# Performance work log

Hardware: AMD Instinct MI355X
Metric: run time of the kernel (lower is better)

Reference implementation:

```python
import jax, jax.numpy as jnp
import numpy as np

CLASSES = 256
SUPERCLASSES = 16
CLASS_FACTOR = CLASSES // SUPERCLASSES
HEIGHT = 448
WIDTH = 160
BATCH = 1
CH_IN = 128
CH_R0 = 256
CH_R1 = 8


def _leaky(v):
    return jnp.where(v >= 0, v, 0.01 * v)


def _grouped1x1(x, W, b):
    # x: (B, H, Cin, W_sp); W: (H, Cout, Cin); b: (H, Cout)
    return jnp.einsum('bhcw,hoc->bhow', x, W) + b[None, :, :, None]


def setup_inputs() -> dict:
    key = jax.random.key(0)
    ks = jax.random.split(key, 16)
    s = 0.05
    return {
        'x_in': jax.random.normal(ks[0], (BATCH, CH_IN, HEIGHT, WIDTH), jnp.float32),
        'W_cl1': jax.random.normal(ks[1], (HEIGHT, 128, CH_IN), jnp.float32) * s,
        'b_cl1': jax.random.normal(ks[2], (HEIGHT, 128), jnp.float32) * s,
        'W_cl2': jax.random.normal(ks[3], (HEIGHT, 128, 128), jnp.float32) * s,
        'b_cl2': jax.random.normal(ks[4], (HEIGHT, 128), jnp.float32) * s,
        'W_cl3': jax.random.normal(ks[5], (HEIGHT, 128, 128), jnp.float32) * s,
        'b_cl3': jax.random.normal(ks[6], (HEIGHT, 128), jnp.float32) * s,
        'W_cl4': jax.random.normal(ks[7], (HEIGHT, CLASSES + 1, 128), jnp.float32) * s,
        'b_cl4': jax.random.normal(ks[8], (HEIGHT, CLASSES + 1), jnp.float32) * s,
        'W_reg1': jax.random.normal(ks[9], (HEIGHT, CH_R0, CH_IN), jnp.float32) * s,
        'b_reg1': jax.random.normal(ks[10], (HEIGHT, CH_R0), jnp.float32) * s,
        'W_cm2': jax.random.normal(ks[11], (SUPERCLASSES * HEIGHT, CH_R0, CH_R1), jnp.float32) * s,
        'b_cm2': jax.random.normal(ks[12], (SUPERCLASSES * HEIGHT, CH_R1), jnp.float32) * s,
        'W_cm3': jax.random.normal(ks[13], (CLASSES * HEIGHT, CH_R1, 1), jnp.float32) * s,
        'b_cm3': jax.random.normal(ks[14], (CLASSES * HEIGHT, 1), jnp.float32) * s,
    }


def reference(x_in, W_cl1, b_cl1, W_cl2, b_cl2, W_cl3, b_cl3, W_cl4, b_cl4,
              W_reg1, b_reg1, W_cm2, b_cm2, W_cm3, b_cm3):
    B, C, H, Wd = x_in.shape
    x = x_in.transpose(0, 2, 1, 3)  # (B, H, C, W) == grouped-conv layout
    x_r = _leaky(_grouped1x1(x, W_reg1, b_reg1))  # (B, H, CH_R0, W)
    # classification branch
    h = _leaky(_grouped1x1(x, W_cl1, b_cl1))
    h = _leaky(_grouped1x1(h, W_cl2, b_cl2))
    h = _leaky(_grouped1x1(h, W_cl3, b_cl3))
    h = _grouped1x1(h, W_cl4, b_cl4)  # (B, H, CLASSES+1, W)
    logits = h.transpose(0, 2, 1, 3)  # (B, CLASSES+1, H, W)
    cls = logits[:, :CLASSES]
    mask = _leaky(logits[:, -1:])  # (B, 1, H, W)
    inds = jnp.argmax(cls, axis=1)[:, None]  # (B, 1, H, W)
    offs = jnp.arange(H)[None, None, :, None]
    # NOTE: original flattens indices in (b, h, w) order...
    inds_r = (inds + offs * CLASSES).reshape(-1).astype(jnp.int32)
    inds_sc = (inds // CLASS_FACTOR + offs * SUPERCLASSES).reshape(-1).astype(jnp.int32)
    # ...while CondMul input rows come in (b, w, h) order (faithful to torch code).
    xr_rows = x_r.transpose(0, 3, 1, 2).reshape(-1, CH_R0)  # (B*W*H, CH_R0)
    y = _leaky(jnp.einsum('nc,nco->no', xr_rows, W_cm2[inds_sc]) + b_cm2[inds_sc])
    r = jnp.einsum('nc,nco->no', y, W_cm3[inds_r]) + b_cm3[inds_r]  # (N, 1)
    r = r.reshape(B, Wd, H, 1).transpose(0, 3, 2, 1)  # (B, 1, H, W)
    x_real = (inds.astype(jnp.float32) + r) * (1.0 / CLASSES)
    return x_real, mask
```

## Files before the change

### kernel.cpp

```cpp
#include <hip/hip_runtime.h>
#include <hip/hip_bf16.h>

#define HH 448
#define WW 160
#define NPIX (HH*WW)

typedef unsigned long long u64;
typedef _Float16 h8 __attribute__((ext_vector_type(8)));
typedef _Float16 h4 __attribute__((ext_vector_type(4)));
typedef float f32x4 __attribute__((ext_vector_type(4)));

#define MFMA16(A,B,C) __builtin_amdgcn_mfma_f32_16x16x32_f16(A,B,C,0,0,0)
#define LO_SCALE 4096.0f
#define LO_INV   (1.0f/4096.0f)

__device__ __forceinline__ float leaky(float v) { return v >= 0.f ? v : 0.01f * v; }

__device__ __forceinline__ u64 packKey(float m, int r) {
    unsigned u = __float_as_uint(m);
    u = (u & 0x80000000u) ? ~u : (u | 0x80000000u);
    return ((u64)u << 32) | (unsigned)(255 - r);
}

__device__ __forceinline__ _Float16 splitHi(float v) { return (_Float16)v; }
__device__ __forceinline__ _Float16 splitLo(float v, _Float16 hi) {
    return (_Float16)((v - (float)hi) * LO_SCALE);
}

__device__ __forceinline__ void cvtA(const float4& v0, const float4& v1, h8& ah, h8& al) {
    const float v[8] = {v0.x,v0.y,v0.z,v0.w,v1.x,v1.y,v1.z,v1.w};
#pragma unroll
    for (int j = 0; j < 8; ++j) {
        const _Float16 hi = splitHi(v[j]);
        ah[j] = hi;
        al[j] = splitLo(v[j], hi);
    }
}

__device__ __forceinline__ void gemmPass(const _Float16* lah, const _Float16* lal,
                                         const float* __restrict__ Wp,
                                         int lrow, int lg, int col0,
                                         f32x4 aH[5], f32x4 aL[5])
{
    const f32x4 zero = {0.f, 0.f, 0.f, 0.f};
#pragma unroll
    for (int c = 0; c < 5; ++c) { aH[c] = zero; aL[c] = zero; }

    const float* wb = Wp + lrow * 128 + lg * 8;
    float4 ca0 = *(const float4*)(wb);
    float4 ca1 = *(const float4*)(wb + 4);
    float4 cb0 = *(const float4*)(wb + 32);
    float4 cb1 = *(const float4*)(wb + 36);

    const int ub = col0 + lrow;

#pragma unroll 1
    for (int s = 0; s < 4; s += 2) {
        const int sa = (s + 2) & 3, sb = (s + 3) & 3;
        float4 na0 = *(const float4*)(wb + sa * 32);
        float4 na1 = *(const float4*)(wb + sa * 32 + 4);
        float4 nb0 = *(const float4*)(wb + sb * 32);
        float4 nb1 = *(const float4*)(wb + sb * 32 + 4);

        h8 Ah, Al;
        cvtA(ca0, ca1, Ah, Al);
        {
            const int gg = (s << 2) + lg;
#pragma unroll
            for (int c = 0; c < 5; ++c) {
                const int u = gg * 160 + ub + (c << 4);
                const h8 Bh = *(const h8*)(lah + (u << 3));
                const h8 Bl = *(const h8*)(lal + (u << 3));
                aH[c] = MFMA16(Ah, Bh, aH[c]);
                aL[c] = MFMA16(Ah, Bl, aL[c]);
                aL[c] = MFMA16(Al, Bh, aL[c]);
            }
        }
        cvtA(cb0, cb1, Ah, Al);
        {
            const int gg = ((s + 1) << 2) + lg;
#pragma unroll
            for (int c = 0; c < 5; ++c) {
                const int u = gg * 160 + ub + (c << 4);
                const h8 Bh = *(const h8*)(lah + (u << 3));
                const h8 Bl = *(const h8*)(lal + (u << 3));
                aH[c] = MFMA16(Ah, Bh, aH[c]);
                aL[c] = MFMA16(Ah, Bl, aL[c]);
                aL[c] = MFMA16(Al, Bh, aL[c]);
            }
        }
        ca0 = na0; ca1 = na1; cb0 = nb0; cb1 = nb1;
    }
}

__global__ __launch_bounds__(1024, 4) void kA(
    const float* __restrict__ x_in,
    const float* __restrict__ Wcl1, const float* __restrict__ bcl1,
    const float* __restrict__ Wcl2, const float* __restrict__ bcl2,
    const float* __restrict__ Wcl3, const float* __restrict__ bcl3,
    const float* __restrict__ Wcl4, const float* __restrict__ bcl4,
    const float* __restrict__ Wreg1, const float* __restrict__ breg1,
    __hip_bfloat16* __restrict__ xr, int* __restrict__ ind, float* __restrict__ out)
{
    __shared__ alignas(16) _Float16 lah[16 * 160 * 8];
    __shared__ alignas(16) _Float16 lal[16 * 160 * 8];
    u64* argb = reinterpret_cast<u64*>(lah);

    const int h = blockIdx.x;
    const int t = threadIdx.x;
    const int wvid = t >> 6;
    const int l = t & 63;
    const int lrow = l & 15, lg = l >> 4;
    const int rt = wvid >> 1;
    const int ch = wvid & 1;
    const int col0 = ch * 80;
    const int trb = rt * 16;

#pragma unroll 1
    for (int k = 0; k < 3; ++k) {
        const int id = t + (k << 10);
        if (id < 2560) {
            const int g = id / 160, col = id - g * 160;
            float v[8];
#pragma unroll
            for (int j = 0; j < 8; ++j)
                v[j] = x_in[(size_t)(g * 8 + j) * 71680 + h * 160 + col];
            h8 hh, ll;
#pragma unroll
            for (int j = 0; j < 8; ++j) {
                const _Float16 hi = splitHi(v[j]);
                hh[j] = hi;
                ll[j] = splitLo(v[j], hi);
            }
            const int u = g * 160 + col;
            *(h8*)(lah + (u << 3)) = hh;
            *(h8*)(lal + (u << 3)) = ll;
        }
    }
    __syncthreads();

    {
        const float* W1 = Wreg1 + (size_t)h * 32768;
        const float* b1 = breg1 + h * 256;
#pragma unroll 1
        for (int p = 0; p < 2; ++p) {
            const int rowOff = (p << 7) + trb;
            f32x4 aH[5], aL[5];
            gemmPass(lah, lal, W1 + rowOff * 128, lrow, lg, col0, aH, aL);
            const int r0 = rowOff + (lg << 2);
            const float4 bb = *(const float4*)&b1[r0];
#pragma unroll
            for (int c = 0; c < 5; ++c) {
                const int col = col0 + (c << 4) + lrow;
                alignas(8) unsigned short us[4];
#pragma unroll
                for (int r = 0; r < 4; ++r) {
                    const float a = aH[c][r] + aL[c][r] * LO_INV + ((const float*)&bb)[r];
                    __hip_bfloat16 bv = __float2bfloat16(leaky(a));
                    us[r] = *(const unsigned short*)&bv;
                }
                *(uint2*)(xr + (((size_t)(h * 160 + col)) << 8) + r0) = *(const uint2*)us;
            }
        }
    }

#pragma unroll 1
    for (int L = 0; L < 3; ++L) {
        const float* W = (L == 0) ? Wcl1 + (size_t)h * 16384
                       : (L == 1) ? Wcl2 + (size_t)h * 16384
                                  : Wcl3 + (size_t)h * 16384;
        const float* b = (L == 0) ? bcl1 + (h << 7)
                       : (L == 1) ? bcl2 + (h << 7)
                                  : bcl3 + (h << 7);
        f32x4 aH[5], aL[5];
        gemmPass(lah, lal, W + trb * 128, lrow, lg, col0, aH, aL);
        const int r0 = trb + (lg << 2);
        const float4 bb = *(const float4*)&b[r0];
        float nv[5][4];
#pragma unroll
        for (int c = 0; c < 5; ++c)
#pragma unroll
            for (int r = 0; r < 4; ++r)
                nv[c][r] = leaky(aH[c][r] + aL[c][r] * LO_INV + ((const float*)&bb)[r]);
        __syncthreads();
        {
            const int g = r0 >> 3, off = r0 & 7;
#pragma unroll
            for (int c = 0; c < 5; ++c) {
                const int col = col0 + (c << 4) + lrow;
                h4 wh, wl;
#pragma unroll
                for (int r = 0; r < 4; ++r) {
                    const _Float16 hi = splitHi(nv[c][r]);
                    wh[r] = hi;
                    wl[r] = splitLo(nv[c][r], hi);
                }
                *(h4*)(lah + ((g * 160 + col) << 3) + off) = wh;
                *(h4*)(lal + ((g * 160 + col) << 3) + off) = wl;
            }
        }
        __syncthreads();
    }

    if (t < 160) {
        const float* Wm = Wcl4 + (size_t)h * 32896 + 32768;
        float accm = 0.f;
#pragma unroll 2
        for (int g = 0; g < 16; ++g) {
            const h8 hv = *(const h8*)(lah + ((g * 160 + t) << 3));
            const h8 lv = *(const h8*)(lal + ((g * 160 + t) << 3));
            const float4 w0 = *(const float4*)&Wm[g * 8];
            const float4 w1 = *(const float4*)&Wm[g * 8 + 4];
            const float wv[8] = {w0.x,w0.y,w0.z,w0.w,w1.x,w1.y,w1.z,w1.w};
#pragma unroll
            for (int j = 0; j < 8; ++j)
                accm = fmaf(wv[j], (float)hv[j] + (float)lv[j] * LO_INV, accm);
        }
        out[NPIX + h * 160 + t] = leaky(accm + bcl4[h * 257 + 256]);
    }

    float mv[5]; int mr[5];
    {
        const float* W4 = Wcl4 + (size_t)h * 32896;
        const float* b4 = bcl4 + h * 257;
#pragma unroll
        for (int c = 0; c < 5; ++c) { mv[c] = -3.4e38f; mr[c] = 0; }
#pragma unroll 1
        for (int p = 0; p < 2; ++p) {
            const int rowOff = (p << 7) + trb;
            f32x4 aH[5], aL[5];
            gemmPass(lah, lal, W4 + rowOff * 128, lrow, lg, col0, aH, aL);
            const int r0 = rowOff + (lg << 2);
            const float4 bb = *(const float4*)&b4[r0];
#pragma unroll
            for (int c = 0; c < 5; ++c)
#pragma unroll
                for (int r = 0; r < 4; ++r) {
                    const float a = aH[c][r] + aL[c][r] * LO_INV + ((const float*)&bb)[r];
                    if (a > mv[c]) { mv[c] = a; mr[c] = r0 + r; }
                }
        }
    }
    __syncthreads();
    if (t < 160) argb[t] = 0ull;
    __syncthreads();
#pragma unroll
    for (int c = 0; c < 5; ++c)
        atomicMax(&argb[col0 + (c << 4) + lrow], packKey(mv[c], mr[c]));
    __syncthreads();

    if (t < 160) {
        const u64 kk = argb[t];
        ind[h * 160 + t] = 255 - (int)(kk & 0xFFu);
    }
}

__global__ __launch_bounds__(256) void kB(
    const __hip_bfloat16* __restrict__ xr, const int* __restrict__ ind,
    const float* __restrict__ Wcm2, const float* __restrict__ bcm2,
    const float* __restrict__ Wcm3, const float* __restrict__ bcm3,
    float* __restrict__ out)
{
    const int wid = (int)((blockIdx.x * blockDim.x + threadIdx.x) >> 6);
    const int lane = threadIdx.x & 63;

#pragma unroll 1
    for (int k = 0; k < 10; ++k) {
        const int n = wid * 10 + k;
        const int h_o = n % HH, w_o = n / HH;
        const int h_i = n / WW, w_i = n % WW;
        const int ig = ind[h_i * WW + w_i];
        const int sc = (ig >> 4) + (h_i << 4);
        const int rr = ig + (h_i << 8);

        const __hip_bfloat16* xp = xr + (size_t)(h_o * WW + w_o) * 256;
        const float* Wp = Wcm2 + (size_t)sc * 2048;

        float acc[8];
#pragma unroll
        for (int o = 0; o < 8; ++o) acc[o] = 0.f;

        const int c0 = lane * 4;
        const ushort4 xv4 = *(const ushort4*)((const unsigned short*)xp + c0);
        float xf[4];
        xf[0] = __uint_as_float((unsigned int)xv4.x << 16);
        xf[1] = __uint_as_float((unsigned int)xv4.y << 16);
        xf[2] = __uint_as_float((unsigned int)xv4.z << 16);
        xf[3] = __uint_as_float((unsigned int)xv4.w << 16);

#pragma unroll
        for (int i = 0; i < 4; ++i) {
            const float4* wrow = (const float4*)&Wp[(c0 + i) * 8];
            const float4 wa = wrow[0];
            const float4 wb_ = wrow[1];
            const float x = xf[i];
            acc[0] += x * wa.x;  acc[1] += x * wa.y;  acc[2] += x * wa.z;  acc[3] += x * wa.w;
            acc[4] += x * wb_.x; acc[5] += x * wb_.y; acc[6] += x * wb_.z; acc[7] += x * wb_.w;
        }
#pragma unroll
        for (int o = 0; o < 8; ++o) {
            float v = acc[o];
#pragma unroll
            for (int d = 32; d > 0; d >>= 1) v += __shfl_xor(v, d, 64);
            acc[o] = v;
        }
        float r = bcm3[rr];
        const float* b2 = bcm2 + (size_t)sc * 8;
        const float* w3 = Wcm3 + (size_t)rr * 8;
#pragma unroll
        for (int o = 0; o < 8; ++o) {
            const float y = leaky(acc[o] + b2[o]);
            r += y * w3[o];
        }
        if (lane == 0) {
            const float iv = (float)ind[h_o * WW + w_o];
            out[h_o * WW + w_o] = (iv + r) * (1.0f / 256.0f);
        }
    }
}

extern "C" void kernel_launch(void* const* d_in, const int* in_sizes, int n_in,
                              void* d_out, int out_size, void* d_ws, size_t ws_size,
                              hipStream_t stream)
{
    const float* x_in  = (const float*)d_in[0];
    const float* Wcl1  = (const float*)d_in[1];
    const float* bcl1  = (const float*)d_in[2];
    const float* Wcl2  = (const float*)d_in[3];
    const float* bcl2  = (const float*)d_in[4];
    const float* Wcl3  = (const float*)d_in[5];
    const float* bcl3  = (const float*)d_in[6];
    const float* Wcl4  = (const float*)d_in[7];
    const float* bcl4  = (const float*)d_in[8];
    const float* Wreg1 = (const float*)d_in[9];
    const float* breg1 = (const float*)d_in[10];
    const float* Wcm2  = (const float*)d_in[11];
    const float* bcm2  = (const float*)d_in[12];
    const float* Wcm3  = (const float*)d_in[13];
    const float* bcm3  = (const float*)d_in[14];

    float* out = (float*)d_out;

    __hip_bfloat16* xr = (__hip_bfloat16*)d_ws;
    int* ind = (int*)((char*)d_ws + (size_t)NPIX * 256 * sizeof(__hip_bfloat16));

    kA<<<dim3(HH), dim3(1024), 0, stream>>>(x_in, Wcl1, bcl1, Wcl2, bcl2, Wcl3, bcl3,
                                            Wcl4, bcl4, Wreg1, breg1, xr, ind, out);
    kB<<<dim3(1792), dim3(256), 0, stream>>>(xr, ind, Wcm2, bcm2, Wcm3, bcm3, out);
}
```

Baseline: 179.0 us.

## Split each row's columns across two 512-thread blocks in kernel A

Kernel A now launches two blocks per height row, each covering 80 of the 160 columns with 8 waves instead of 16, and halves the shared-memory buffers. Block IDs are remapped so that paired halves of neighbouring rows are scheduled together. This gives 896 blocks instead of 448, which should fill the 256 CUs more evenly and let more blocks share a CU through the smaller LDS footprint. The cost is that each block re-reads the full per-row weight matrices, doubling weight traffic from L2/HBM.

```diff
diff --git a/kernel.cpp b/kernel.cpp
--- a/kernel.cpp
+++ b/kernel.cpp
@@ -4,6 +4,7 @@
 #define HH 448
 #define WW 160
 #define NPIX (HH*WW)
+#define BCOL 80
 
 typedef unsigned long long u64;
 typedef _Float16 h8 __attribute__((ext_vector_type(8)));
@@ -39,7 +40,7 @@
 
 __device__ __forceinline__ void gemmPass(const _Float16* lah, const _Float16* lal,
                                          const float* __restrict__ Wp,
-                                         int lrow, int lg, int col0,
+                                         int lrow, int lg,
                                          f32x4 aH[5], f32x4 aL[5])
 {
     const f32x4 zero = {0.f, 0.f, 0.f, 0.f};
@@ -52,7 +53,7 @@
     float4 cb0 = *(const float4*)(wb + 32);
     float4 cb1 = *(const float4*)(wb + 36);
 
-    const int ub = col0 + lrow;
+    const int ub = lrow;
 
 #pragma unroll 1
     for (int s = 0; s < 4; s += 2) {
@@ -68,7 +69,7 @@
             const int gg = (s << 2) + lg;
 #pragma unroll
             for (int c = 0; c < 5; ++c) {
-                const int u = gg * 160 + ub + (c << 4);
+                const int u = gg * BCOL + ub + (c << 4);
                 const h8 Bh = *(const h8*)(lah + (u << 3));
                 const h8 Bl = *(const h8*)(lal + (u << 3));
                 aH[c] = MFMA16(Ah, Bh, aH[c]);
@@ -81,7 +82,7 @@
             const int gg = ((s + 1) << 2) + lg;
 #pragma unroll
             for (int c = 0; c < 5; ++c) {
-                const int u = gg * 160 + ub + (c << 4);
+                const int u = gg * BCOL + ub + (c << 4);
                 const h8 Bh = *(const h8*)(lah + (u << 3));
                 const h8 Bl = *(const h8*)(lal + (u << 3));
                 aH[c] = MFMA16(Ah, Bh, aH[c]);
@@ -93,7 +94,7 @@
     }
 }
 
-__global__ __launch_bounds__(1024, 4) void kA(
+__global__ __launch_bounds__(512, 4) void kA(
     const float* __restrict__ x_in,
     const float* __restrict__ Wcl1, const float* __restrict__ bcl1,
     const float* __restrict__ Wcl2, const float* __restrict__ bcl2,
@@ -102,29 +103,30 @@
     const float* __restrict__ Wreg1, const float* __restrict__ breg1,
     __hip_bfloat16* __restrict__ xr, int* __restrict__ ind, float* __restrict__ out)
 {
-    __shared__ alignas(16) _Float16 lah[16 * 160 * 8];
-    __shared__ alignas(16) _Float16 lal[16 * 160 * 8];
+    __shared__ alignas(16) _Float16 lah[16 * BCOL * 8];
+    __shared__ alignas(16) _Float16 lal[16 * BCOL * 8];
     u64* argb = reinterpret_cast<u64*>(lah);
 
-    const int h = blockIdx.x;
+    const int bid = blockIdx.x;
+    const int r16 = bid & 15;
+    const int h = ((bid >> 4) << 3) | (r16 & 7);
+    const int w0 = ((r16 >> 3) & 1) * BCOL;
+
     const int t = threadIdx.x;
     const int wvid = t >> 6;
     const int l = t & 63;
     const int lrow = l & 15, lg = l >> 4;
-    const int rt = wvid >> 1;
-    const int ch = wvid & 1;
-    const int col0 = ch * 80;
-    const int trb = rt * 16;
+    const int trb = wvid * 16;
 
 #pragma unroll 1
     for (int k = 0; k < 3; ++k) {
-        const int id = t + (k << 10);
-        if (id < 2560) {
-            const int g = id / 160, col = id - g * 160;
+        const int id = t + (k << 9);
+        if (id < 16 * BCOL) {
+            const int g = id / BCOL, col = id - g * BCOL;
             float v[8];
 #pragma unroll
             for (int j = 0; j < 8; ++j)
-                v[j] = x_in[(size_t)(g * 8 + j) * 71680 + h * 160 + col];
+                v[j] = x_in[(size_t)(g * 8 + j) * 71680 + h * 160 + w0 + col];
             h8 hh, ll;
 #pragma unroll
             for (int j = 0; j < 8; ++j) {
@@ -132,7 +134,7 @@
                 hh[j] = hi;
                 ll[j] = splitLo(v[j], hi);
             }
-            const int u = g * 160 + col;
+            const int u = g * BCOL + col;
             *(h8*)(lah + (u << 3)) = hh;
             *(h8*)(lal + (u << 3)) = ll;
         }
@@ -146,12 +148,12 @@
         for (int p = 0; p < 2; ++p) {
             const int rowOff = (p << 7) + trb;
             f32x4 aH[5], aL[5];
-            gemmPass(lah, lal, W1 + rowOff * 128, lrow, lg, col0, aH, aL);
+            gemmPass(lah, lal, W1 + rowOff * 128, lrow, lg, aH, aL);
             const int r0 = rowOff + (lg << 2);
             const float4 bb = *(const float4*)&b1[r0];
 #pragma unroll
             for (int c = 0; c < 5; ++c) {
-                const int col = col0 + (c << 4) + lrow;
+                const int col = w0 + (c << 4) + lrow;
                 alignas(8) unsigned short us[4];
 #pragma unroll
                 for (int r = 0; r < 4; ++r) {
@@ -173,50 +175,50 @@
                        : (L == 1) ? bcl2 + (h << 7)
                                   : bcl3 + (h << 7);
         f32x4 aH[5], aL[5];
-        gemmPass(lah, lal, W + trb * 128, lrow, lg, col0, aH, aL);
+        gemmPass(lah, lal, W + trb * 128, lrow, lg, aH, aL);
         const int r0 = trb + (lg << 2);
         const float4 bb = *(const float4*)&b[r0];
         float nv[5][4];
 #pragma unroll
         for (int c = 0; c < 5; ++c)
 #pragma unroll
-            for (int r = 0; r < 4; ++r)
-                nv[c][r] = leaky(aH[c][r] + aL[c][r] * LO_INV + ((const float*)&bb)[r]);
+            for (int rr = 0; rr < 4; ++rr)
+                nv[c][rr] = leaky(aH[c][rr] + aL[c][rr] * LO_INV + ((const float*)&bb)[rr]);
         __syncthreads();
         {
             const int g = r0 >> 3, off = r0 & 7;
 #pragma unroll
             for (int c = 0; c < 5; ++c) {
-                const int col = col0 + (c << 4) + lrow;
+                const int col = (c << 4) + lrow;
                 h4 wh, wl;
 #pragma unroll
-                for (int r = 0; r < 4; ++r) {
-                    const _Float16 hi = splitHi(nv[c][r]);
-                    wh[r] = hi;
-                    wl[r] = splitLo(nv[c][r], hi);
+                for (int rr = 0; rr < 4; ++rr) {
+                    const _Float16 hi = splitHi(nv[c][rr]);
+                    wh[rr] = hi;
+                    wl[rr] = splitLo(nv[c][rr], hi);
                 }
-                *(h4*)(lah + ((g * 160 + col) << 3) + off) = wh;
-                *(h4*)(lal + ((g * 160 + col) << 3) + off) = wl;
+                *(h4*)(lah + ((g * BCOL + col) << 3) + off) = wh;
+                *(h4*)(lal + ((g * BCOL + col) << 3) + off) = wl;
             }
         }
         __syncthreads();
     }
 
-    if (t < 160) {
+    if (t < BCOL) {
         const float* Wm = Wcl4 + (size_t)h * 32896 + 32768;
         float accm = 0.f;
 #pragma unroll 2
         for (int g = 0; g < 16; ++g) {
-            const h8 hv = *(const h8*)(lah + ((g * 160 + t) << 3));
-            const h8 lv = *(const h8*)(lal + ((g * 160 + t) << 3));
-            const float4 w0 = *(const float4*)&Wm[g * 8];
-            const float4 w1 = *(const float4*)&Wm[g * 8 + 4];
-            const float wv[8] = {w0.x,w0.y,w0.z,w0.w,w1.x,w1.y,w1.z,w1.w};
+            const h8 hv = *(const h8*)(lah + ((g * BCOL + t) << 3));
+            const h8 lv = *(const h8*)(lal + ((g * BCOL + t) << 3));
+            const float4 wv0 = *(const float4*)&Wm[g * 8];
+            const float4 wv1 = *(const float4*)&Wm[g * 8 + 4];
+            const float wv[8] = {wv0.x,wv0.y,wv0.z,wv0.w,wv1.x,wv1.y,wv1.z,wv1.w};
 #pragma unroll
             for (int j = 0; j < 8; ++j)
                 accm = fmaf(wv[j], (float)hv[j] + (float)lv[j] * LO_INV, accm);
         }
-        out[NPIX + h * 160 + t] = leaky(accm + bcl4[h * 257 + 256]);
+        out[NPIX + h * 160 + w0 + t] = leaky(accm + bcl4[h * 257 + 256]);
     }
 
     float mv[5]; int mr[5];
@@ -229,29 +231,29 @@
         for (int p = 0; p < 2; ++p) {
             const int rowOff = (p << 7) + trb;
             f32x4 aH[5], aL[5];
-            gemmPass(lah, lal, W4 + rowOff * 128, lrow, lg, col0, aH, aL);
+            gemmPass(lah, lal, W4 + rowOff * 128, lrow, lg, aH, aL);
             const int r0 = rowOff + (lg << 2);
             const float4 bb = *(const float4*)&b4[r0];
 #pragma unroll
             for (int c = 0; c < 5; ++c)
 #pragma unroll
-                for (int r = 0; r < 4; ++r) {
-                    const float a = aH[c][r] + aL[c][r] * LO_INV + ((const float*)&bb)[r];
-                    if (a > mv[c]) { mv[c] = a; mr[c] = r0 + r; }
+                for (int rr = 0; rr < 4; ++rr) {
+                    const float a = aH[c][rr] + aL[c][rr] * LO_INV + ((const float*)&bb)[rr];
+                    if (a > mv[c]) { mv[c] = a; mr[c] = r0 + rr; }
                 }
         }
     }
     __syncthreads();
-    if (t < 160) argb[t] = 0ull;
+    if (t < BCOL) argb[t] = 0ull;
     __syncthreads();
 #pragma unroll
     for (int c = 0; c < 5; ++c)
-        atomicMax(&argb[col0 + (c << 4) + lrow], packKey(mv[c], mr[c]));
+        atomicMax(&argb[(c << 4) + lrow], packKey(mv[c], mr[c]));
     __syncthreads();
 
-    if (t < 160) {
+    if (t < BCOL) {
         const u64 kk = argb[t];
-        ind[h * 160 + t] = 255 - (int)(kk & 0xFFu);
+        ind[h * 160 + w0 + t] = 255 - (int)(kk & 0xFFu);
     }
 }
 
@@ -344,7 +346,7 @@
     __hip_bfloat16* xr = (__hip_bfloat16*)d_ws;
     int* ind = (int*)((char*)d_ws + (size_t)NPIX * 256 * sizeof(__hip_bfloat16));
 
-    kA<<<dim3(HH), dim3(1024), 0, stream>>>(x_in, Wcl1, bcl1, Wcl2, bcl2, Wcl3, bcl3,
-                                            Wcl4, bcl4, Wreg1, breg1, xr, ind, out);
+    kA<<<dim3(HH * 2), dim3(512), 0, stream>>>(x_in, Wcl1, bcl1, Wcl2, bcl2, Wcl3, bcl3,
+                                               Wcl4, bcl4, Wreg1, breg1, xr, ind, out);
     kB<<<dim3(1792), dim3(256), 0, stream>>>(xr, ind, Wcm2, bcm2, Wcm3, bcm3, out);
 }
```

New measurement: 176.9 us. No clear change (-1.2%).
